# Performance work log

Hardware: AMD Instinct MI355X
Metric: run time of the kernel (lower is better)

## Reference

```python
import jax, jax.numpy as jnp
import numpy as np

B = 131072
H_GAS = 8
H_EXT = 16
# gas order and net counts, total 99 tiny MLPs
GAS_SIZES = [23, 29, 13, 9, 3, 9, 13]  # h2o, h2o_sq, o3, co2, n2o, ch4, u
N_NETS = 29

# index maps taken verbatim from the 29 tau_gases assignment lines
H2O_ROWS = np.arange(23)
H2O_IDX = np.array([0,1,2,3,4,5,6,3,4,9,10,11,12,13,14,15,16,17,18,19,20,21,22])
O3_ROWS = np.array([0,1,2,17,18,19,20,21,22,25,26,27,28])
CO2_ROWS = np.array([0,1,2,5,6,9,10,13,14])
N2O_ROWS = np.array([0,1,2])
CH4_ROWS = np.array([0,1,2,3,4,7,8,11,12])
U_ROWS = np.array([0,1,2,15,16,17,18,19,20,21,22,27,28])


def setup_inputs() -> dict:
    key = jax.random.key(0)
    ks = jax.random.split(key, 23)
    f = jnp.float32
    inp = {
        'temp': jax.random.normal(ks[0], (B, 1), f),
        'pressure': jax.random.normal(ks[1], (B, 1), f),
        'comp_h2o': jax.random.uniform(ks[2], (B, 1), f),
        'comp_h2o_sq': jax.random.uniform(ks[3], (B, 1), f),
        'comp_o3': jax.random.uniform(ks[4], (B, 1), f),
        'comp_co2': jax.random.uniform(ks[5], (B, 1), f),
        'comp_n2o': jax.random.uniform(ks[6], (B, 1), f),
        'comp_ch4': jax.random.uniform(ks[7], (B, 1), f),
        'comp_u': jax.random.uniform(ks[8], (B, 1), f),
        'lwp': jax.random.uniform(ks[9], (B, 1), f, minval=0.05, maxval=1.0),
        'iwp': jax.random.uniform(ks[10], (B, 1), f, minval=0.05, maxval=1.0),
        'mu': jax.random.uniform(ks[11], (B, 1), f, minval=0.1, maxval=1.0),
        'mu_bar': jax.random.uniform(ks[12], (B, 1), f, minval=0.1, maxval=1.0),
        'gas_W1': jax.random.normal(ks[13], (99, 2, H_GAS), f) * 0.5,
        'gas_b1': jax.random.normal(ks[14], (99, H_GAS), f) * 0.1,
        'gas_W2': jax.random.normal(ks[15], (99, H_GAS, 1), f) * 0.5,
        'gas_b2': jax.random.uniform(ks[16], (99, 1), f, minval=0.05, maxval=0.5),
        'lw_w': jax.random.uniform(ks[17], (N_NETS, 1), f, minval=0.05, maxval=1.0),
        'iw_w': jax.random.uniform(ks[18], (N_NETS, 1), f, minval=0.05, maxval=1.0),
        'ext_W1': jax.random.normal(ks[19], (N_NETS, 4, H_EXT), f) * 0.5,
        'ext_b1': jax.random.normal(ks[20], (N_NETS, H_EXT), f) * 0.1,
        'ext_W2': jax.random.normal(ks[21], (N_NETS, H_EXT, 3), f) * 0.5,
        'ext_b2': jax.random.normal(ks[22], (N_NETS, 3), f) * 0.1,
    }
    return inp


def reference(temp, pressure, comp_h2o, comp_h2o_sq, comp_o3, comp_co2, comp_n2o,
              comp_ch4, comp_u, lwp, iwp, mu, mu_bar,
              gas_W1, gas_b1, gas_W2, gas_b2, lw_w, iw_w,
              ext_W1, ext_b1, ext_W2, ext_b2):
    b = temp.shape[0]
    X = jnp.concatenate([temp, pressure], axis=-1)              # [B,2]
    # all 99 per-gas tiny MLPs in one batched pass
    h = jax.nn.elu(jnp.einsum('bi,nih->nbh', X, gas_W1) + gas_b1[:, None, :])
    ke = jax.nn.relu(jnp.einsum('nbh,nho->nbo', h, gas_W2) + gas_b2[:, None, :])[..., 0]  # [99,B]
    comps = [comp_h2o, comp_h2o_sq, comp_o3, comp_co2, comp_n2o, comp_ch4, comp_u]
    comp_all = jnp.concatenate(
        [jnp.broadcast_to(c[:, 0][None, :], (n, b)) for c, n in zip(comps, GAS_SIZES)], axis=0)
    tau_all = ke * comp_all                                      # [99,B]
    h2o    = tau_all[0:23]
    h2o_sq = tau_all[23:52]
    o3     = tau_all[52:65]
    co2    = tau_all[65:74]
    n2o    = tau_all[74:77]
    ch4    = tau_all[77:86]
    u      = tau_all[86:99]
    # scatter-combine into the 29 spectral channels
    tau_g = h2o_sq                                               # every row has h2o_sq[k]
    tau_g = tau_g.at[H2O_ROWS].add(h2o[H2O_IDX])
    tau_g = tau_g.at[O3_ROWS].add(o3)
    tau_g = tau_g.at[CO2_ROWS].add(co2)
    tau_g = tau_g.at[N2O_ROWS].add(n2o)
    tau_g = tau_g.at[CH4_ROWS].add(ch4)
    tau_g = tau_g.at[U_ROWS].add(u)
    tau_lw = lw_w * lwp[:, 0][None, :]                           # [29,B]
    tau_iw = iw_w * iwp[:, 0][None, :]
    tau_total = tau_g + tau_lw + tau_iw
    in1 = tau_lw / tau_total
    in2 = tau_iw / tau_total
    mu_v, mub_v = mu[:, 0], mu_bar[:, 0]
    in3_dir = tau_total / mu_v[None, :]
    in3_dif = tau_total / mub_v[None, :]

    def ext(i1, i2, i3, m):
        Xe = jnp.stack([i1, i2, i3, jnp.broadcast_to(m[None, :], i1.shape)], axis=-1)  # [29,B,4]
        he = jax.nn.elu(jnp.einsum('nbi,nih->nbh', Xe, ext_W1) + ext_b1[:, None, :])
        return jax.nn.relu(jnp.einsum('nbh,nho->nbo', he, ext_W2) + ext_b2[:, None, :])

    e_direct = jax.nn.softmax(ext(in1, in2, in3_dir, mu_v), axis=-1)   # [29,B,3]
    e_diffuse = jax.nn.softmax(ext(in1, in2, in3_dif, mub_v), axis=-1)
    t_direct = jnp.exp(-in3_dir)
    t_diffuse = jnp.exp(-in3_dif)
    return (t_direct, t_diffuse, e_direct, e_diffuse)
```

## Files before the change

### kernel.cpp

```cpp
#include <hip/hip_runtime.h>
#include <math.h>

#define TPB 256

static __device__ const int ROW_START[30] = {
    0, 7, 14, 21, 24, 27, 30, 33, 36, 39, 42, 45, 48, 51, 54, 57, 60,
    63, 67, 71, 75, 79, 83, 87, 88, 89, 91, 93, 96, 99};

static __device__ const unsigned char NET_ID[99] = {
    23, 0, 52, 65, 74, 77, 86,
    24, 1, 53, 66, 75, 78, 87,
    25, 2, 54, 67, 76, 79, 88,
    26, 3, 80,
    27, 4, 81,
    28, 5, 68,
    29, 6, 69,
    30, 3, 82,
    31, 4, 83,
    32, 9, 70,
    33, 10, 71,
    34, 11, 84,
    35, 12, 85,
    36, 13, 72,
    37, 14, 73,
    38, 15, 89,
    39, 16, 90,
    40, 17, 55, 91,
    41, 18, 56, 92,
    42, 19, 57, 93,
    43, 20, 58, 94,
    44, 21, 59, 95,
    45, 22, 60, 96,
    46,
    47,
    48, 61,
    49, 62,
    50, 63, 97,
    51, 64, 98};

static __device__ const unsigned char COMP_ID[99] = {
    1, 0, 2, 3, 4, 5, 6,
    1, 0, 2, 3, 4, 5, 6,
    1, 0, 2, 3, 4, 5, 6,
    1, 0, 5,
    1, 0, 5,
    1, 0, 3,
    1, 0, 3,
    1, 0, 5,
    1, 0, 5,
    1, 0, 3,
    1, 0, 3,
    1, 0, 5,
    1, 0, 5,
    1, 0, 3,
    1, 0, 3,
    1, 0, 6,
    1, 0, 6,
    1, 0, 2, 6,
    1, 0, 2, 6,
    1, 0, 2, 6,
    1, 0, 2, 6,
    1, 0, 2, 6,
    1, 0, 2, 6,
    1,
    1,
    1, 2,
    1, 2,
    1, 2, 6,
    1, 2, 6};

__device__ __forceinline__ float fast_rcp(float x) {
    return __builtin_amdgcn_rcpf(x);
}

__global__ __launch_bounds__(TPB) void atm_kernel(
    const float* __restrict__ temp,
    const float* __restrict__ pressure,
    const float* __restrict__ c_h2o,
    const float* __restrict__ c_h2o_sq,
    const float* __restrict__ c_o3,
    const float* __restrict__ c_co2,
    const float* __restrict__ c_n2o,
    const float* __restrict__ c_ch4,
    const float* __restrict__ c_u,
    const float* __restrict__ lwp,
    const float* __restrict__ iwp,
    const float* __restrict__ mu,
    const float* __restrict__ mu_bar,
    const float* __restrict__ gW1,
    const float* __restrict__ gb1,
    const float* __restrict__ gW2,
    const float* __restrict__ gb2,
    const float* __restrict__ lw_w,
    const float* __restrict__ iw_w,
    const float* __restrict__ eW1,
    const float* __restrict__ eb1,
    const float* __restrict__ eW2,
    const float* __restrict__ eb2,
    float* __restrict__ out,
    int Bn)
{
    const int r = blockIdx.x;
    const int b = blockIdx.y * TPB + threadIdx.x;
    if (b >= Bn) return;

    const float t = temp[b];
    const float p = pressure[b];
    float comp[7];
    comp[0] = c_h2o[b];
    comp[1] = c_h2o_sq[b];
    comp[2] = c_o3[b];
    comp[3] = c_co2[b];
    comp[4] = c_n2o[b];
    comp[5] = c_ch4[b];
    comp[6] = c_u[b];
    const float lwp_b = lwp[b], iwp_b = iwp[b];
    const float mu_b = mu[b], mub_b = mu_bar[b];

    float tau_g = 0.f;
    const int i0 = ROW_START[r], i1 = ROW_START[r + 1];
    for (int i = i0; i < i1; ++i) {
        const int n = NET_ID[i];
        const float* w1 = gW1 + n * 16;
        const float* b1 = gb1 + n * 8;
        const float* w2 = gW2 + n * 8;
        float acc = gb2[n];
        #pragma unroll
        for (int j = 0; j < 8; ++j) {
            float h = fmaf(t, w1[j], fmaf(p, w1[8 + j], b1[j]));
            h = h > 0.f ? h : (__expf(h) - 1.f);
            acc = fmaf(h, w2[j], acc);
        }
        acc = fmaxf(acc, 0.f);
        tau_g = fmaf(acc, comp[COMP_ID[i]], tau_g);
    }

    const float tlw = lw_w[r] * lwp_b;
    const float tiw = iw_w[r] * iwp_b;
    const float tau_tot = tau_g + tlw + tiw;
    const float inv_tt = fast_rcp(tau_tot);
    const float in1 = tlw * inv_tt;
    const float in2 = tiw * inv_tt;
    const float in3_dir = tau_tot * fast_rcp(mu_b);
    const float in3_dif = tau_tot * fast_rcp(mub_b);

    const size_t idx = (size_t)r * (size_t)Bn + (size_t)b;
    out[idx] = __expf(-in3_dir);
    out[(size_t)29 * Bn + idx] = __expf(-in3_dif);

    const float* w1 = eW1 + r * 64;
    const float* b1 = eb1 + r * 16;
    const float* w2 = eW2 + r * 48;
    const float* b2 = eb2 + r * 3;

    float res[6];
    #pragma unroll
    for (int pass = 0; pass < 2; ++pass) {
        const float i3 = (pass == 0) ? in3_dir : in3_dif;
        const float m  = (pass == 0) ? mu_b : mub_b;
        float o0 = b2[0], o1 = b2[1], o2 = b2[2];
        #pragma unroll
        for (int j = 0; j < 16; ++j) {
            float h = fmaf(in1, w1[j], b1[j]);
            h = fmaf(in2, w1[16 + j], h);
            h = fmaf(i3,  w1[32 + j], h);
            h = fmaf(m,   w1[48 + j], h);
            h = h > 0.f ? h : (__expf(h) - 1.f);
            o0 = fmaf(h, w2[3 * j + 0], o0);
            o1 = fmaf(h, w2[3 * j + 1], o1);
            o2 = fmaf(h, w2[3 * j + 2], o2);
        }
        o0 = fmaxf(o0, 0.f);
        o1 = fmaxf(o1, 0.f);
        o2 = fmaxf(o2, 0.f);
        const float mx = fmaxf(o0, fmaxf(o1, o2));
        const float e0 = __expf(o0 - mx);
        const float e1 = __expf(o1 - mx);
        const float e2 = __expf(o2 - mx);
        const float rs = fast_rcp(e0 + e1 + e2);
        res[pass * 3 + 0] = e0 * rs;
        res[pass * 3 + 1] = e1 * rs;
        res[pass * 3 + 2] = e2 * rs;
    }

    float* pd = out + (size_t)58 * Bn + idx * 3;
    pd[0] = res[0]; pd[1] = res[1]; pd[2] = res[2];
    float* pf = out + (size_t)145 * Bn + idx * 3;
    pf[0] = res[3]; pf[1] = res[4]; pf[2] = res[5];
}

extern "C" void kernel_launch(void* const* d_in, const int* in_sizes, int n_in,
                              void* d_out, int out_size, void* d_ws, size_t ws_size,
                              hipStream_t stream) {
    const int Bn = in_sizes[0];
    dim3 grid(29, (Bn + TPB - 1) / TPB);
    atm_kernel<<<grid, TPB, 0, stream>>>(
        (const float*)d_in[0],  (const float*)d_in[1],  (const float*)d_in[2],
        (const float*)d_in[3],  (const float*)d_in[4],  (const float*)d_in[5],
        (const float*)d_in[6],  (const float*)d_in[7],  (const float*)d_in[8],
        (const float*)d_in[9],  (const float*)d_in[10], (const float*)d_in[11],
        (const float*)d_in[12], (const float*)d_in[13], (const float*)d_in[14],
        (const float*)d_in[15], (const float*)d_in[16], (const float*)d_in[17],
        (const float*)d_in[18], (const float*)d_in[19], (const float*)d_in[20],
        (const float*)d_in[21], (const float*)d_in[22],
        (float*)d_out, Bn);
}
```

Measured before the change: 227.2 us.

## Process four batch elements per thread with vectorized loads and stores

```diff
diff --git a/kernel.cpp b/kernel.cpp
--- a/kernel.cpp
+++ b/kernel.cpp
@@ -2,6 +2,7 @@
 #include <math.h>
 
 #define TPB 256
+#define EPT 4
 
 static __device__ const int ROW_START[30] = {
     0, 7, 14, 21, 24, 27, 30, 33, 36, 39, 42, 45, 48, 51, 54, 57, 60,
@@ -73,6 +74,20 @@
     return __builtin_amdgcn_rcpf(x);
 }
 
+__device__ __forceinline__ void load4(const float* __restrict__ p, long long b0,
+                                      int Bn, bool full, float v[EPT]) {
+    if (full) {
+        const float4 q = *(const float4*)(p + b0);
+        v[0] = q.x; v[1] = q.y; v[2] = q.z; v[3] = q.w;
+    } else {
+        #pragma unroll
+        for (int e = 0; e < EPT; ++e) {
+            long long b = b0 + e;
+            v[e] = p[b < Bn ? b : (Bn - 1)];
+        }
+    }
+}
+
 __global__ __launch_bounds__(TPB) void atm_kernel(
     const float* __restrict__ temp,
     const float* __restrict__ pressure,
@@ -101,99 +116,193 @@
     int Bn)
 {
     const int r = blockIdx.x;
-    const int b = blockIdx.y * TPB + threadIdx.x;
-    if (b >= Bn) return;
-
-    const float t = temp[b];
-    const float p = pressure[b];
-    float comp[7];
-    comp[0] = c_h2o[b];
-    comp[1] = c_h2o_sq[b];
-    comp[2] = c_o3[b];
-    comp[3] = c_co2[b];
-    comp[4] = c_n2o[b];
-    comp[5] = c_ch4[b];
-    comp[6] = c_u[b];
-    const float lwp_b = lwp[b], iwp_b = iwp[b];
-    const float mu_b = mu[b], mub_b = mu_bar[b];
-
-    float tau_g = 0.f;
+    const long long vb = (long long)blockIdx.y * TPB + threadIdx.x;
+    const long long b0 = vb * EPT;
+    if (b0 >= Bn) return;
+    const bool full = (b0 + EPT <= Bn);
+
+    float t_[EPT], p_[EPT];
+    float cm0[EPT], cm1[EPT], cm2[EPT], cm3[EPT], cm4[EPT], cm5[EPT], cm6[EPT];
+    float lwp_[EPT], iwp_[EPT], mu_[EPT], mub_[EPT];
+    load4(temp,      b0, Bn, full, t_);
+    load4(pressure,  b0, Bn, full, p_);
+    load4(c_h2o,     b0, Bn, full, cm0);
+    load4(c_h2o_sq,  b0, Bn, full, cm1);
+    load4(c_o3,      b0, Bn, full, cm2);
+    load4(c_co2,     b0, Bn, full, cm3);
+    load4(c_n2o,     b0, Bn, full, cm4);
+    load4(c_ch4,     b0, Bn, full, cm5);
+    load4(c_u,       b0, Bn, full, cm6);
+    load4(lwp,       b0, Bn, full, lwp_);
+    load4(iwp,       b0, Bn, full, iwp_);
+    load4(mu,        b0, Bn, full, mu_);
+    load4(mu_bar,    b0, Bn, full, mub_);
+
+    float tG[EPT] = {0.f, 0.f, 0.f, 0.f};
     const int i0 = ROW_START[r], i1 = ROW_START[r + 1];
     for (int i = i0; i < i1; ++i) {
-        const int n = NET_ID[i];
-        const float* w1 = gW1 + n * 16;
-        const float* b1 = gb1 + n * 8;
-        const float* w2 = gW2 + n * 8;
-        float acc = gb2[n];
+        const int n   = NET_ID[i];
+        const int cid = COMP_ID[i];
+        const float* w1  = gW1 + n * 16;
+        const float* bb1 = gb1 + n * 8;
+        const float* w2  = gW2 + n * 8;
+        const float bias2 = gb2[n];
+        float acc[EPT];
+        #pragma unroll
+        for (int e = 0; e < EPT; ++e) acc[e] = bias2;
         #pragma unroll
         for (int j = 0; j < 8; ++j) {
-            float h = fmaf(t, w1[j], fmaf(p, w1[8 + j], b1[j]));
-            h = h > 0.f ? h : (__expf(h) - 1.f);
-            acc = fmaf(h, w2[j], acc);
-        }
-        acc = fmaxf(acc, 0.f);
-        tau_g = fmaf(acc, comp[COMP_ID[i]], tau_g);
-    }
-
-    const float tlw = lw_w[r] * lwp_b;
-    const float tiw = iw_w[r] * iwp_b;
-    const float tau_tot = tau_g + tlw + tiw;
-    const float inv_tt = fast_rcp(tau_tot);
-    const float in1 = tlw * inv_tt;
-    const float in2 = tiw * inv_tt;
-    const float in3_dir = tau_tot * fast_rcp(mu_b);
-    const float in3_dif = tau_tot * fast_rcp(mub_b);
-
-    const size_t idx = (size_t)r * (size_t)Bn + (size_t)b;
-    out[idx] = __expf(-in3_dir);
-    out[(size_t)29 * Bn + idx] = __expf(-in3_dif);
-
-    const float* w1 = eW1 + r * 64;
-    const float* b1 = eb1 + r * 16;
-    const float* w2 = eW2 + r * 48;
-    const float* b2 = eb2 + r * 3;
-
-    float res[6];
+            const float a0  = w1[j];
+            const float a1  = w1[8 + j];
+            const float bj  = bb1[j];
+            const float w2j = w2[j];
+            #pragma unroll
+            for (int e = 0; e < EPT; ++e) {
+                float h = fmaf(t_[e], a0, fmaf(p_[e], a1, bj));
+                h = h > 0.f ? h : (__expf(h) - 1.f);
+                acc[e] = fmaf(h, w2j, acc[e]);
+            }
+        }
+        float cv[EPT];
+        switch (cid) {
+            case 0:
+                for (int e = 0; e < EPT; ++e) cv[e] = cm0[e];
+                break;
+            case 1:
+                for (int e = 0; e < EPT; ++e) cv[e] = cm1[e];
+                break;
+            case 2:
+                for (int e = 0; e < EPT; ++e) cv[e] = cm2[e];
+                break;
+            case 3:
+                for (int e = 0; e < EPT; ++e) cv[e] = cm3[e];
+                break;
+            case 4:
+                for (int e = 0; e < EPT; ++e) cv[e] = cm4[e];
+                break;
+            case 5:
+                for (int e = 0; e < EPT; ++e) cv[e] = cm5[e];
+                break;
+            default:
+                for (int e = 0; e < EPT; ++e) cv[e] = cm6[e];
+                break;
+        }
+        #pragma unroll
+        for (int e = 0; e < EPT; ++e)
+            tG[e] = fmaf(fmaxf(acc[e], 0.f), cv[e], tG[e]);
+    }
+
+    const float lwr = lw_w[r], iwr = iw_w[r];
+    float in1[EPT], in2[EPT], i3d[EPT], i3f[EPT], td[EPT], tf[EPT];
     #pragma unroll
-    for (int pass = 0; pass < 2; ++pass) {
-        const float i3 = (pass == 0) ? in3_dir : in3_dif;
-        const float m  = (pass == 0) ? mu_b : mub_b;
-        float o0 = b2[0], o1 = b2[1], o2 = b2[2];
-        #pragma unroll
-        for (int j = 0; j < 16; ++j) {
-            float h = fmaf(in1, w1[j], b1[j]);
-            h = fmaf(in2, w1[16 + j], h);
-            h = fmaf(i3,  w1[32 + j], h);
-            h = fmaf(m,   w1[48 + j], h);
-            h = h > 0.f ? h : (__expf(h) - 1.f);
-            o0 = fmaf(h, w2[3 * j + 0], o0);
-            o1 = fmaf(h, w2[3 * j + 1], o1);
-            o2 = fmaf(h, w2[3 * j + 2], o2);
-        }
-        o0 = fmaxf(o0, 0.f);
-        o1 = fmaxf(o1, 0.f);
-        o2 = fmaxf(o2, 0.f);
-        const float mx = fmaxf(o0, fmaxf(o1, o2));
-        const float e0 = __expf(o0 - mx);
-        const float e1 = __expf(o1 - mx);
-        const float e2 = __expf(o2 - mx);
-        const float rs = fast_rcp(e0 + e1 + e2);
-        res[pass * 3 + 0] = e0 * rs;
-        res[pass * 3 + 1] = e1 * rs;
-        res[pass * 3 + 2] = e2 * rs;
-    }
-
-    float* pd = out + (size_t)58 * Bn + idx * 3;
-    pd[0] = res[0]; pd[1] = res[1]; pd[2] = res[2];
-    float* pf = out + (size_t)145 * Bn + idx * 3;
-    pf[0] = res[3]; pf[1] = res[4]; pf[2] = res[5];
+    for (int e = 0; e < EPT; ++e) {
+        const float tlw = lwr * lwp_[e];
+        const float tiw = iwr * iwp_[e];
+        const float tt  = tG[e] + tlw + tiw;
+        const float inv = fast_rcp(tt);
+        in1[e] = tlw * inv;
+        in2[e] = tiw * inv;
+        i3d[e] = tt * fast_rcp(mu_[e]);
+        i3f[e] = tt * fast_rcp(mub_[e]);
+        td[e]  = __expf(-i3d[e]);
+        tf[e]  = __expf(-i3f[e]);
+    }
+
+    const float* w1  = eW1 + r * 64;
+    const float* bb1 = eb1 + r * 16;
+    const float* w2  = eW2 + r * 48;
+    const float b20 = eb2[r * 3 + 0], b21 = eb2[r * 3 + 1], b22 = eb2[r * 3 + 2];
+
+    float o[2][EPT][3];
+    #pragma unroll
+    for (int pp = 0; pp < 2; ++pp)
+        #pragma unroll
+        for (int e = 0; e < EPT; ++e) {
+            o[pp][e][0] = b20; o[pp][e][1] = b21; o[pp][e][2] = b22;
+        }
+
+    #pragma unroll
+    for (int j = 0; j < 16; ++j) {
+        const float wj0 = w1[j];
+        const float wj1 = w1[16 + j];
+        const float wj2 = w1[32 + j];
+        const float wj3 = w1[48 + j];
+        const float bj  = bb1[j];
+        const float u0 = w2[3 * j + 0];
+        const float u1 = w2[3 * j + 1];
+        const float u2 = w2[3 * j + 2];
+        #pragma unroll
+        for (int e = 0; e < EPT; ++e) {
+            const float base = fmaf(in1[e], wj0, fmaf(in2[e], wj1, bj));
+            {
+                float h = fmaf(mu_[e], wj3, fmaf(i3d[e], wj2, base));
+                h = h > 0.f ? h : (__expf(h) - 1.f);
+                o[0][e][0] = fmaf(h, u0, o[0][e][0]);
+                o[0][e][1] = fmaf(h, u1, o[0][e][1]);
+                o[0][e][2] = fmaf(h, u2, o[0][e][2]);
+            }
+            {
+                float h = fmaf(mub_[e], wj3, fmaf(i3f[e], wj2, base));
+                h = h > 0.f ? h : (__expf(h) - 1.f);
+                o[1][e][0] = fmaf(h, u0, o[1][e][0]);
+                o[1][e][1] = fmaf(h, u1, o[1][e][1]);
+                o[1][e][2] = fmaf(h, u2, o[1][e][2]);
+            }
+        }
+    }
+
+    float sm[2][EPT][3];
+    #pragma unroll
+    for (int pp = 0; pp < 2; ++pp)
+        #pragma unroll
+        for (int e = 0; e < EPT; ++e) {
+            const float a0 = fmaxf(o[pp][e][0], 0.f);
+            const float a1 = fmaxf(o[pp][e][1], 0.f);
+            const float a2 = fmaxf(o[pp][e][2], 0.f);
+            const float mx = fmaxf(a0, fmaxf(a1, a2));
+            const float e0 = __expf(a0 - mx);
+            const float e1 = __expf(a1 - mx);
+            const float e2 = __expf(a2 - mx);
+            const float rs = fast_rcp(e0 + e1 + e2);
+            sm[pp][e][0] = e0 * rs;
+            sm[pp][e][1] = e1 * rs;
+            sm[pp][e][2] = e2 * rs;
+        }
+
+    const size_t Bn4 = (size_t)Bn >> 2;
+    if (full) {
+        float4* o4 = (float4*)out;
+        o4[(size_t)r * Bn4 + vb]        = make_float4(td[0], td[1], td[2], td[3]);
+        o4[(size_t)(29 + r) * Bn4 + vb] = make_float4(tf[0], tf[1], tf[2], tf[3]);
+        float4* pd = (float4*)(out + (size_t)Bn * (58 + 3 * (size_t)r)) + 3 * vb;
+        pd[0] = make_float4(sm[0][0][0], sm[0][0][1], sm[0][0][2], sm[0][1][0]);
+        pd[1] = make_float4(sm[0][1][1], sm[0][1][2], sm[0][2][0], sm[0][2][1]);
+        pd[2] = make_float4(sm[0][2][2], sm[0][3][0], sm[0][3][1], sm[0][3][2]);
+        float4* pf = (float4*)(out + (size_t)Bn * (145 + 3 * (size_t)r)) + 3 * vb;
+        pf[0] = make_float4(sm[1][0][0], sm[1][0][1], sm[1][0][2], sm[1][1][0]);
+        pf[1] = make_float4(sm[1][1][1], sm[1][1][2], sm[1][2][0], sm[1][2][1]);
+        pf[2] = make_float4(sm[1][2][2], sm[1][3][0], sm[1][3][1], sm[1][3][2]);
+    } else {
+        #pragma unroll
+        for (int e = 0; e < EPT; ++e) {
+            const long long b = b0 + e;
+            if (b >= Bn) break;
+            const size_t idx = (size_t)r * Bn + (size_t)b;
+            out[idx] = td[e];
+            out[(size_t)29 * Bn + idx] = tf[e];
+            float* pd = out + (size_t)58 * Bn + idx * 3;
+            pd[0] = sm[0][e][0]; pd[1] = sm[0][e][1]; pd[2] = sm[0][e][2];
+            float* pf = out + (size_t)145 * Bn + idx * 3;
+            pf[0] = sm[1][e][0]; pf[1] = sm[1][e][1]; pf[2] = sm[1][e][2];
+        }
+    }
 }
 
 extern "C" void kernel_launch(void* const* d_in, const int* in_sizes, int n_in,
                               void* d_out, int out_size, void* d_ws, size_t ws_size,
                               hipStream_t stream) {
     const int Bn = in_sizes[0];
-    dim3 grid(29, (Bn + TPB - 1) / TPB);
+    dim3 grid(29, (Bn + TPB * EPT - 1) / (TPB * EPT));
     atm_kernel<<<grid, TPB, 0, stream>>>(
         (const float*)d_in[0],  (const float*)d_in[1],  (const float*)d_in[2],
         (const float*)d_in[3],  (const float*)d_in[4],  (const float*)d_in[5],
```

Result: slower. 235.3 us (+3.5%).

## Specialize gas rows at compile time, share ext first layer, and swap grid axes

Applied to the files above, without the earlier changes.

```diff
diff --git a/kernel.cpp b/kernel.cpp
--- a/kernel.cpp
+++ b/kernel.cpp
@@ -3,11 +3,11 @@
 
 #define TPB 256
 
-static __device__ const int ROW_START[30] = {
+constexpr int ROW_START[30] = {
     0, 7, 14, 21, 24, 27, 30, 33, 36, 39, 42, 45, 48, 51, 54, 57, 60,
     63, 67, 71, 75, 79, 83, 87, 88, 89, 91, 93, 96, 99};
 
-static __device__ const unsigned char NET_ID[99] = {
+constexpr int NET_ID[99] = {
     23, 0, 52, 65, 74, 77, 86,
     24, 1, 53, 66, 75, 78, 87,
     25, 2, 54, 67, 76, 79, 88,
@@ -38,7 +38,7 @@
     50, 63, 97,
     51, 64, 98};
 
-static __device__ const unsigned char COMP_ID[99] = {
+constexpr int COMP_ID[99] = {
     1, 0, 2, 3, 4, 5, 6,
     1, 0, 2, 3, 4, 5, 6,
     1, 0, 2, 3, 4, 5, 6,
@@ -71,6 +71,35 @@
 
 __device__ __forceinline__ float fast_rcp(float x) {
     return __builtin_amdgcn_rcpf(x);
+}
+
+__device__ __forceinline__ float elu(float h) {
+    return fmaxf(h, __expf(fminf(h, 0.f)) - 1.f);
+}
+
+template <int R>
+__device__ __forceinline__ float gas_row(
+    float t, float p, const float* comp,
+    const float* __restrict__ gW1, const float* __restrict__ gb1,
+    const float* __restrict__ gW2, const float* __restrict__ gb2)
+{
+    float tg = 0.f;
+    #pragma unroll
+    for (int i = ROW_START[R]; i < ROW_START[R + 1]; ++i) {
+        const int n = NET_ID[i];
+        const float c = comp[COMP_ID[i]];
+        const float* w1 = gW1 + n * 16;
+        const float* b1 = gb1 + n * 8;
+        const float* w2 = gW2 + n * 8;
+        float acc = gb2[n];
+        #pragma unroll
+        for (int j = 0; j < 8; ++j) {
+            float h = fmaf(t, w1[j], fmaf(p, w1[8 + j], b1[j]));
+            acc = fmaf(elu(h), w2[j], acc);
+        }
+        tg = fmaf(fmaxf(acc, 0.f), c, tg);
+    }
+    return tg;
 }
 
 __global__ __launch_bounds__(TPB) void atm_kernel(
@@ -100,8 +129,8 @@
     float* __restrict__ out,
     int Bn)
 {
-    const int r = blockIdx.x;
-    const int b = blockIdx.y * TPB + threadIdx.x;
+    const int r = blockIdx.y;
+    const long long b = (long long)blockIdx.x * TPB + threadIdx.x;
     if (b >= Bn) return;
 
     const float t = temp[b];
@@ -118,21 +147,16 @@
     const float mu_b = mu[b], mub_b = mu_bar[b];
 
     float tau_g = 0.f;
-    const int i0 = ROW_START[r], i1 = ROW_START[r + 1];
-    for (int i = i0; i < i1; ++i) {
-        const int n = NET_ID[i];
-        const float* w1 = gW1 + n * 16;
-        const float* b1 = gb1 + n * 8;
-        const float* w2 = gW2 + n * 8;
-        float acc = gb2[n];
-        #pragma unroll
-        for (int j = 0; j < 8; ++j) {
-            float h = fmaf(t, w1[j], fmaf(p, w1[8 + j], b1[j]));
-            h = h > 0.f ? h : (__expf(h) - 1.f);
-            acc = fmaf(h, w2[j], acc);
-        }
-        acc = fmaxf(acc, 0.f);
-        tau_g = fmaf(acc, comp[COMP_ID[i]], tau_g);
+    switch (r) {
+#define ROW_CASE(R) case R: tau_g = gas_row<R>(t, p, comp, gW1, gb1, gW2, gb2); break;
+        ROW_CASE(0)  ROW_CASE(1)  ROW_CASE(2)  ROW_CASE(3)  ROW_CASE(4)
+        ROW_CASE(5)  ROW_CASE(6)  ROW_CASE(7)  ROW_CASE(8)  ROW_CASE(9)
+        ROW_CASE(10) ROW_CASE(11) ROW_CASE(12) ROW_CASE(13) ROW_CASE(14)
+        ROW_CASE(15) ROW_CASE(16) ROW_CASE(17) ROW_CASE(18) ROW_CASE(19)
+        ROW_CASE(20) ROW_CASE(21) ROW_CASE(22) ROW_CASE(23) ROW_CASE(24)
+        ROW_CASE(25) ROW_CASE(26) ROW_CASE(27) ROW_CASE(28)
+#undef ROW_CASE
+        default: break;
     }
 
     const float tlw = lw_w[r] * lwp_b;
@@ -148,52 +172,61 @@
     out[idx] = __expf(-in3_dir);
     out[(size_t)29 * Bn + idx] = __expf(-in3_dif);
 
-    const float* w1 = eW1 + r * 64;
-    const float* b1 = eb1 + r * 16;
-    const float* w2 = eW2 + r * 48;
-    const float* b2 = eb2 + r * 3;
-
-    float res[6];
+    const float* w1  = eW1 + r * 64;
+    const float* bb1 = eb1 + r * 16;
+    const float* w2  = eW2 + r * 48;
+    const float b20 = eb2[r * 3 + 0], b21 = eb2[r * 3 + 1], b22 = eb2[r * 3 + 2];
+
+    float od0 = b20, od1 = b21, od2 = b22;
+    float of0 = b20, of1 = b21, of2 = b22;
     #pragma unroll
-    for (int pass = 0; pass < 2; ++pass) {
-        const float i3 = (pass == 0) ? in3_dir : in3_dif;
-        const float m  = (pass == 0) ? mu_b : mub_b;
-        float o0 = b2[0], o1 = b2[1], o2 = b2[2];
-        #pragma unroll
-        for (int j = 0; j < 16; ++j) {
-            float h = fmaf(in1, w1[j], b1[j]);
-            h = fmaf(in2, w1[16 + j], h);
-            h = fmaf(i3,  w1[32 + j], h);
-            h = fmaf(m,   w1[48 + j], h);
-            h = h > 0.f ? h : (__expf(h) - 1.f);
-            o0 = fmaf(h, w2[3 * j + 0], o0);
-            o1 = fmaf(h, w2[3 * j + 1], o1);
-            o2 = fmaf(h, w2[3 * j + 2], o2);
+    for (int j = 0; j < 16; ++j) {
+        const float wj0 = w1[j];
+        const float wj1 = w1[16 + j];
+        const float wj2 = w1[32 + j];
+        const float wj3 = w1[48 + j];
+        const float bj  = bb1[j];
+        const float u0 = w2[3 * j + 0];
+        const float u1 = w2[3 * j + 1];
+        const float u2 = w2[3 * j + 2];
+        const float base = fmaf(in1, wj0, fmaf(in2, wj1, bj));
+        {
+            const float h = elu(fmaf(mu_b, wj3, fmaf(in3_dir, wj2, base)));
+            od0 = fmaf(h, u0, od0);
+            od1 = fmaf(h, u1, od1);
+            od2 = fmaf(h, u2, od2);
         }
-        o0 = fmaxf(o0, 0.f);
-        o1 = fmaxf(o1, 0.f);
-        o2 = fmaxf(o2, 0.f);
-        const float mx = fmaxf(o0, fmaxf(o1, o2));
-        const float e0 = __expf(o0 - mx);
-        const float e1 = __expf(o1 - mx);
-        const float e2 = __expf(o2 - mx);
+        {
+            const float h = elu(fmaf(mub_b, wj3, fmaf(in3_dif, wj2, base)));
+            of0 = fmaf(h, u0, of0);
+            of1 = fmaf(h, u1, of1);
+            of2 = fmaf(h, u2, of2);
+        }
+    }
+
+    float* pd = out + (size_t)58 * Bn + idx * 3;
+    {
+        const float a0 = fmaxf(od0, 0.f), a1 = fmaxf(od1, 0.f), a2 = fmaxf(od2, 0.f);
+        const float mx = fmaxf(a0, fmaxf(a1, a2));
+        const float e0 = __expf(a0 - mx), e1 = __expf(a1 - mx), e2 = __expf(a2 - mx);
         const float rs = fast_rcp(e0 + e1 + e2);
-        res[pass * 3 + 0] = e0 * rs;
-        res[pass * 3 + 1] = e1 * rs;
-        res[pass * 3 + 2] = e2 * rs;
-    }
-
-    float* pd = out + (size_t)58 * Bn + idx * 3;
-    pd[0] = res[0]; pd[1] = res[1]; pd[2] = res[2];
+        pd[0] = e0 * rs; pd[1] = e1 * rs; pd[2] = e2 * rs;
+    }
     float* pf = out + (size_t)145 * Bn + idx * 3;
-    pf[0] = res[3]; pf[1] = res[4]; pf[2] = res[5];
+    {
+        const float a0 = fmaxf(of0, 0.f), a1 = fmaxf(of1, 0.f), a2 = fmaxf(of2, 0.f);
+        const float mx = fmaxf(a0, fmaxf(a1, a2));
+        const float e0 = __expf(a0 - mx), e1 = __expf(a1 - mx), e2 = __expf(a2 - mx);
+        const float rs = fast_rcp(e0 + e1 + e2);
+        pf[0] = e0 * rs; pf[1] = e1 * rs; pf[2] = e2 * rs;
+    }
 }
 
 extern "C" void kernel_launch(void* const* d_in, const int* in_sizes, int n_in,
                               void* d_out, int out_size, void* d_ws, size_t ws_size,
                               hipStream_t stream) {
     const int Bn = in_sizes[0];
-    dim3 grid(29, (Bn + TPB - 1) / TPB);
+    dim3 grid((Bn + TPB - 1) / TPB, 29);
     atm_kernel<<<grid, TPB, 0, stream>>>(
         (const float*)d_in[0],  (const float*)d_in[1],  (const float*)d_in[2],
         (const float*)d_in[3],  (const float*)d_in[4],  (const float*)d_in[5],
```

New measurement: 230.4 us. Within noise of the previous version (+1.4%).
